# Performance work log

Hardware: AMD Instinct MI355X
Metric: run time of the kernel (lower is better)

## Reference

```python
import jax, jax.numpy as jnp
import numpy as np

N, E, G = 20000, 640000, 64
D_IN, H, C, D_OUT = 256, 4, 64, 32
HC = H * C


def gat_layer(x, W, a_src, a_dst, b, src, dst, n_nodes, heads, ch):
    # x: [N, F_in], W: [F_in, H*C]
    h = (x @ W).reshape(n_nodes, heads, ch)          # [N,H,C]
    es = jnp.einsum('nhc,hc->nh', h, a_src)          # [N,H]
    ed = jnp.einsum('nhc,hc->nh', h, a_dst)
    e = jax.nn.leaky_relu(es[src] + ed[dst], 0.2)    # [Etot,H]
    m = jax.ops.segment_max(e, dst, num_segments=n_nodes)
    m = jnp.where(jnp.isfinite(m), m, 0.0)
    ex = jnp.exp(e - m[dst])
    denom = jax.ops.segment_sum(ex, dst, num_segments=n_nodes)
    alpha = ex / jnp.maximum(denom[dst], 1e-16)      # softmax over in-edges per dst
    out = jax.ops.segment_sum(alpha[:, :, None] * h[src], dst, num_segments=n_nodes)
    return out.reshape(n_nodes, heads * ch) + b


def setup_inputs() -> dict:
    key = jax.random.key(0)
    ks = jax.random.split(key, 14)
    g1 = 1.0 / np.sqrt(D_IN)
    g2 = 1.0 / np.sqrt(HC)
    inp = {
        'x': jax.random.normal(ks[0], (N, D_IN), jnp.float32),
        'edge_index': jax.random.randint(ks[1], (2, E), 0, N, jnp.int64 if jax.config.jax_enable_x64 else jnp.int32),
        'batch': jnp.sort(jax.random.randint(ks[2], (N,), 0, G)),
        'W1': jax.random.normal(ks[3], (D_IN, HC), jnp.float32) * g1,
        'a_src1': jax.random.normal(ks[4], (H, C), jnp.float32) * g2,
        'a_dst1': jax.random.normal(ks[5], (H, C), jnp.float32) * g2,
        'b1': jnp.zeros((HC,), jnp.float32),
        'W2': jax.random.normal(ks[6], (HC, HC), jnp.float32) * g2,
        'a_src2': jax.random.normal(ks[7], (H, C), jnp.float32) * g2,
        'a_dst2': jax.random.normal(ks[8], (H, C), jnp.float32) * g2,
        'b2': jnp.zeros((HC,), jnp.float32),
        'Wp': jax.random.normal(ks[9], (HC, D_OUT), jnp.float32) * g2,
        'bp': jnp.zeros((D_OUT,), jnp.float32),
    }
    return inp


def reference(x, edge_index, batch, W1, a_src1, a_dst1, b1, W2, a_src2, a_dst2, b2, Wp, bp):
    # add self-loops (PyG GATConv default)
    loop = jnp.arange(N, dtype=edge_index.dtype)
    src = jnp.concatenate([edge_index[0], loop])
    dst = jnp.concatenate([edge_index[1], loop])
    x1 = jax.nn.relu(gat_layer(x, W1, a_src1, a_dst1, b1, src, dst, N, H, C))
    # dropout p=0.6 is identity in eval mode
    x2 = jax.nn.relu(gat_layer(x1, W2, a_src2, a_dst2, b2, src, dst, N, H, C))
    node_scores = x2 @ Wp + bp                        # [N, D_OUT]
    sums = jax.ops.segment_sum(node_scores, batch, num_segments=G)
    counts = jax.ops.segment_sum(jnp.ones((N,), node_scores.dtype), batch, num_segments=G)
    return sums / jnp.maximum(counts, 1.0)[:, None]   # [G, D_OUT]
```

## Files before the change

kernel.cpp:

```cpp
#include <hip/hip_runtime.h>
#include <hip/hip_bf16.h>
#include <cstdint>

#define NNODES 20000
#define NEDGES 640000
#define ETOT   (NEDGES + NNODES)
#define NGROUP 64
#define HC     256
#define DOUT   32
#define EBLK   5120
#define NBLK   125
#define CBLK   79
#define GBLK   1250
#define ABLK   2500

typedef short bf16x8 __attribute__((ext_vector_type(8)));
typedef short s16x4  __attribute__((ext_vector_type(4)));
typedef float f32x4  __attribute__((ext_vector_type(4)));
typedef float f32x2  __attribute__((ext_vector_type(2)));
typedef int   s32x4  __attribute__((ext_vector_type(4)));
typedef unsigned int u32x4 __attribute__((ext_vector_type(4)));

__device__ __forceinline__ float bs2f(short v) {
    union { unsigned int u; float f; } c; c.u = ((unsigned int)(unsigned short)v) << 16; return c.f;
}
__device__ __forceinline__ short f2bs(float v) {
    __hip_bfloat16 b = __float2bfloat16(v);
    union { __hip_bfloat16 b; short s; } u; u.b = b; return u.s;
}
__device__ __forceinline__ float ldf(const void* __restrict__ p, size_t i, int bf) {
    return bf ? __bfloat162float(((const __hip_bfloat16*)p)[i]) : ((const float*)p)[i];
}
__device__ __forceinline__ int ld_idx(const int* __restrict__ p, size_t i, int f64) {
    return f64 ? p[2 * i] : p[i];
}
__device__ __forceinline__ unsigned enc_f(float f) {
    unsigned u = __float_as_uint(f);
    return (u >> 31) ? ~u : (u | 0x80000000u);
}
__device__ __forceinline__ float dec_f(unsigned e) {
    return (e >> 31) ? __uint_as_float(e & 0x7FFFFFFFu) : __uint_as_float(~e);
}
__device__ __forceinline__ int probe_edge64(const int* __restrict__ ei) {
    int l = threadIdx.x & 63;
    int zeros = 0;
#pragma unroll
    for (int r = 0; r < 4; r++)
        zeros += __popcll(__ballot(ei[2 * (r * 64 + l) + 1] == 0));
    return (zeros > 200) ? 1 : 0;
}
__device__ __forceinline__ int probe_xbf(const unsigned int* __restrict__ xw) {
    int l = threadIdx.x & 63;
    int ones = 0;
#pragma unroll
    for (int r = 0; r < 4; r++)
        ones += __popcll(__ballot((xw[r * 64 + l] >> 14) & 1));
    return (ones < 64) ? 1 : 0;
}
__device__ __forceinline__ void signal_done(int* ctr) {
    __threadfence();
    __syncthreads();
    if (threadIdx.x == 0) atomicAdd(ctr, 1);
}
__device__ __forceinline__ void spin_wait(int* ctr, int target) {
    if (threadIdx.x == 0) {
        while (__hip_atomic_load(ctr, __ATOMIC_RELAXED, __HIP_MEMORY_SCOPE_AGENT) < target)
            __builtin_amdgcn_s_sleep(8);
    }
    __syncthreads();
    __threadfence();
}

__global__ __launch_bounds__(256) void k_setup(const unsigned int* __restrict__ xw,
                                               const int* __restrict__ ei,
                                               const int* __restrict__ bat,
                                               const void* __restrict__ W1, const void* __restrict__ W2,
                                               __hip_bfloat16* __restrict__ Wt1,
                                               __hip_bfloat16* __restrict__ Wt2,
                                               int* __restrict__ H,
                                               float* __restrict__ sx, int* __restrict__ cnt,
                                               unsigned* __restrict__ gp2, int* __restrict__ sy) {
    __shared__ int hl[NNODES];
    int t = threadIdx.x, b = blockIdx.x;
    if (b < NBLK) {
        int f = probe_edge64(ei);
        s32x4* hl4 = reinterpret_cast<s32x4*>(hl);
        for (int i = t; i < NNODES / 4; i += 256) hl4[i] = (s32x4){0, 0, 0, 0};
        __syncthreads();
        int s0 = b * EBLK;
        if (f) {
            const int* d64 = ei + 2 * NEDGES;
            for (int i0 = s0; i0 < s0 + EBLK; i0 += 512) {
                int i = i0 + 2 * t;
                s32x4 v = *reinterpret_cast<const s32x4*>(d64 + 2 * (size_t)i);
                atomicAdd(&hl[v[0]], 1);
                atomicAdd(&hl[v[2]], 1);
            }
        } else {
            const int* d32 = ei + NEDGES;
            for (int i0 = s0; i0 < s0 + EBLK; i0 += 1024) {
                int i = i0 + 4 * t;
                s32x4 v = *reinterpret_cast<const s32x4*>(d32 + i);
                atomicAdd(&hl[v[0]], 1); atomicAdd(&hl[v[1]], 1);
                atomicAdd(&hl[v[2]], 1); atomicAdd(&hl[v[3]], 1);
            }
        }
        __syncthreads();
        s32x4* Hb4 = reinterpret_cast<s32x4*>(H + (size_t)b * NNODES);
        for (int i = t; i < NNODES / 4; i += 256) Hb4[i] = hl4[i];
    } else {
        int bf = probe_xbf(xw);
        int i = (b - NBLK) * 256 + t;
        int which = i >> 16;
        int j = i & 65535;
        int k = j >> 8, n = j & 255;
        const void* W = which ? W2 : W1;
        __hip_bfloat16* Wt = which ? Wt2 : Wt1;
        Wt[(size_t)n * 256 + k] = __float2bfloat16(ldf(W, (size_t)k * 256 + n, bf));
        if (b == NBLK) {
            for (int q = t; q < NGROUP * HC; q += 256) sx[q] = 0.f;
            if (t < 256) gp2[t] = 0x007FFFFFu;
            if (t < 8) sy[t] = 0;
            int f = probe_edge64(ei);
            if (t < NGROUP) hl[t] = 0;
            __syncthreads();
            for (int r = t; r < NNODES; r += 256) atomicAdd(&hl[ld_idx(bat, r, f)], 1);
            __syncthreads();
            if (t < NGROUP) cnt[t] = hl[t];
        }
    }
}

__device__ __forceinline__ void dev_gemm(int tile, const void* __restrict__ A,
                                         const __hip_bfloat16* __restrict__ Bt,
                                         __hip_bfloat16* __restrict__ Hout,
                                         const void* __restrict__ a_src, const void* __restrict__ a_dst,
                                         float* __restrict__ es4, float* __restrict__ ed4,
                                         unsigned* __restrict__ gp2, int bf, int abf,
                                         u32x4* hst4) {
    int w    = threadIdx.x >> 6;
    int lane = threadIdx.x & 63;
    int mr   = lane & 15;
    int quad = lane >> 4;
    int r0   = tile * 16;
    f32x4 acc[4];
#pragma unroll
    for (int j = 0; j < 4; j++) acc[j] = (f32x4){0.f, 0.f, 0.f, 0.f};
    size_t rowoff = (size_t)(r0 + mr) * HC;
    const __hip_bfloat16* Btw = Bt + (size_t)w * 64 * HC;
    for (int kk = 0; kk < HC; kk += 32) {
        bf16x8 a;
        if (abf) {
            a = *reinterpret_cast<const bf16x8*>((const __hip_bfloat16*)A + rowoff + kk + quad * 8);
        } else {
            const float* af = (const float*)A + rowoff + kk + quad * 8;
            f32x4 lo = *reinterpret_cast<const f32x4*>(af);
            f32x4 hi = *reinterpret_cast<const f32x4*>(af + 4);
#pragma unroll
            for (int ii = 0; ii < 4; ii++) { a[ii] = f2bs(lo[ii]); a[ii + 4] = f2bs(hi[ii]); }
        }
#pragma unroll
        for (int j = 0; j < 4; j++) {
            bf16x8 b = *reinterpret_cast<const bf16x8*>(Btw + (size_t)(j * 16 + mr) * HC + kk + quad * 8);
            acc[j] = __builtin_amdgcn_mfma_f32_16x16x32_bf16(a, b, acc[j], 0, 0, 0);
        }
    }
    short* hst = reinterpret_cast<short*>(hst4);
#pragma unroll
    for (int j = 0; j < 4; j++)
#pragma unroll
        for (int r = 0; r < 4; r++)
            hst[(quad * 4 + r) * HC + w * 64 + j * 16 + mr] = f2bs(acc[j][r]);
    float ps[4] = {0.f, 0.f, 0.f, 0.f}, pd[4] = {0.f, 0.f, 0.f, 0.f};
#pragma unroll
    for (int j = 0; j < 4; j++) {
        float asv = ldf(a_src, (size_t)(w * 64 + j * 16 + mr), bf);
        float adv = ldf(a_dst, (size_t)(w * 64 + j * 16 + mr), bf);
#pragma unroll
        for (int r = 0; r < 4; r++) {
            ps[r] = fmaf(acc[j][r], asv, ps[r]);
            pd[r] = fmaf(acc[j][r], adv, pd[r]);
        }
    }
#pragma unroll
    for (int o = 1; o < 16; o <<= 1)
#pragma unroll
        for (int r = 0; r < 4; r++) {
            ps[r] += __shfl_xor(ps[r], o);
            pd[r] += __shfl_xor(pd[r], o);
        }
    float pm = fmaxf(fmaxf(ps[0], ps[1]), fmaxf(ps[2], ps[3]));
    pm = fmaxf(pm, __shfl_xor(pm, 16));
    pm = fmaxf(pm, __shfl_xor(pm, 32));
    if (lane == 0) atomicMax(&gp2[w * 64 + (tile & 63)], enc_f(pm));
    if (mr == 0)
#pragma unroll
        for (int r = 0; r < 4; r++) {
            int row = r0 + quad * 4 + r;
            es4[(size_t)row * 4 + w] = ps[r];
            ed4[(size_t)row * 4 + w] = pd[r];
        }
    __syncthreads();
    u32x4* dst = reinterpret_cast<u32x4*>((short*)Hout + (size_t)r0 * HC);
    dst[threadIdx.x]       = hst4[threadIdx.x];
    dst[threadIdx.x + 256] = hst4[threadIdx.x + 256];
}

__global__ __launch_bounds__(256) void k_p2(const void* __restrict__ x,
                                            const int* __restrict__ ei,
                                            int* __restrict__ H, int* __restrict__ bsum,
                                            int* __restrict__ off, int* __restrict__ csr,
                                            const __hip_bfloat16* __restrict__ Wt1,
                                            __hip_bfloat16* __restrict__ hb,
                                            const void* __restrict__ as1, const void* __restrict__ ad1,
                                            float* __restrict__ es, float* __restrict__ ed,
                                            unsigned* __restrict__ gp2, int* __restrict__ sy) {
    __shared__ int smem[2048];
    int bid = blockIdx.x, t = threadIdx.x;
    if (bid < CBLK) {
        int n = bid * 256 + t;
        int lane = t & 63, w = t >> 6;
        int d = 0;
        if (n < NNODES) {
#pragma unroll 5
            for (int b = 0; b < NBLK; b++) d += H[(size_t)b * NNODES + n];
            d += 1;
        }
        int r = d;
#pragma unroll
        for (int o = 1; o < 64; o <<= 1) r += __shfl_xor(r, o);
        if (lane == 0) smem[w] = r;
        __syncthreads();
        if (t == 0) bsum[bid] = smem[0] + smem[1] + smem[2] + smem[3];
        signal_done(&sy[0]);
        spin_wait(&sy[0], CBLK);
        int sc = d;
#pragma unroll
        for (int o = 1; o < 64; o <<= 1) {
            int u = __shfl_up(sc, o);
            if (lane >= o) sc += u;
        }
        if (lane == 63) smem[w] = sc;
        if (w == 0) {
            int v = (lane < bid) ? bsum[lane] : 0;
            if (lane + 64 < bid) v += bsum[lane + 64];
#pragma unroll
            for (int o = 1; o < 64; o <<= 1) v += __shfl_xor(v, o);
            if (lane == 0) smem[4] = v;
        }
        __syncthreads();
        int woff = 0;
        for (int i = 0; i < w; i++) woff += smem[i];
        int excl = woff + sc - d;
        if (bid == 0 && t == 0) off[NNODES] = ETOT;
        if (n < NNODES) {
            int o0 = smem[4] + excl;
            off[n] = o0;
            csr[o0] = n;
            int run = o0 + 1;
#pragma unroll 5
            for (int b = 0; b < NBLK; b++) {
                size_t idx = (size_t)b * NNODES + n;
                int tt = H[idx];
                H[idx] = run;
                run += tt;
            }
        }
        signal_done(&sy[1]);
    } else if (bid < CBLK + NBLK) {
        int b = bid - CBLK;
        int f = probe_edge64(ei);
        spin_wait(&sy[1], CBLK);
        int* Hb = H + (size_t)b * NNODES;
        int s0 = b * EBLK;
        if (f) {
            const int* d64 = ei + 2 * NEDGES;
            for (int i0 = s0; i0 < s0 + EBLK; i0 += 512) {
                int i = i0 + 2 * t;
                s32x4 sv = *reinterpret_cast<const s32x4*>(ei + 2 * (size_t)i);
                s32x4 dv = *reinterpret_cast<const s32x4*>(d64 + 2 * (size_t)i);
                int p0 = atomicAdd(&Hb[dv[0]], 1); csr[p0] = sv[0];
                int p1 = atomicAdd(&Hb[dv[2]], 1); csr[p1] = sv[2];
            }
        } else {
            const int* d32 = ei + NEDGES;
            for (int i0 = s0; i0 < s0 + EBLK; i0 += 1024) {
                int i = i0 + 4 * t;
                s32x4 sv = *reinterpret_cast<const s32x4*>(ei + i);
                s32x4 dv = *reinterpret_cast<const s32x4*>(d32 + i);
#pragma unroll
                for (int k = 0; k < 4; k++) {
                    int p = atomicAdd(&Hb[dv[k]], 1); csr[p] = sv[k];
                }
            }
        }
    } else {
        int bf = probe_xbf((const unsigned int*)x);
        dev_gemm(bid - (CBLK + NBLK), x, Wt1, hb, as1, ad1, es, ed, gp2, bf, bf,
                 (u32x4*)smem);
    }
}

__global__ __launch_bounds__(256) void k_agg(const void* __restrict__ x,
                                             const __hip_bfloat16* __restrict__ Hb,
                                             const float* __restrict__ es4, const float* __restrict__ ed4,
                                             const void* __restrict__ bias,
                                             const int* __restrict__ off, const int* __restrict__ csr,
                                             const unsigned* __restrict__ gp2,
                                             __hip_bfloat16* __restrict__ out) {
    __shared__ float p_lds[4][4][64];
    __shared__ int   s_lds[4][64];
    __shared__ float gm_s[4];
    int wv = threadIdx.x >> 6;
    int l  = threadIdx.x & 63;
    int half = l >> 5;
    int hl   = l & 31;
    int hd8  = hl >> 3;
    int bf = probe_xbf((const unsigned int*)x);
    {
        float m = dec_f(gp2[wv * 64 + l]);
#pragma unroll
        for (int o = 32; o; o >>= 1) m = fmaxf(m, __shfl_xor(m, o));
        if (l == 0) gm_s[wv] = m;
    }
    __syncthreads();
    f32x4 gm = (f32x4){gm_s[0], gm_s[1], gm_s[2], gm_s[3]};
    int n0 = blockIdx.x * 4 + wv;
    for (int n = n0; n < NNODES; n += 10000) {
        int base = off[n], deg = off[n + 1] - base;
        f32x4 edv = *reinterpret_cast<const f32x4*>(ed4 + (size_t)n * 4);
        f32x4 M;
#pragma unroll
        for (int h = 0; h < 4; h++) {
            float t0 = gm[h] + edv[h];
            M[h] = (t0 > 0.f) ? t0 : 0.2f * t0;
        }
        f32x4 dsum = (f32x4){0.f, 0.f, 0.f, 0.f};
        f32x2 acc2[4];
#pragma unroll
        for (int d = 0; d < 4; d++) acc2[d] = (f32x2){0.f, 0.f};
        for (int c0 = 0; c0 < deg; c0 += 64) {
            int cn = min(deg - c0, 64);
            int s = 0;
            f32x4 pv = (f32x4){0.f, 0.f, 0.f, 0.f};
            if (l < cn) {
                s = csr[base + c0 + l];
                f32x4 e = *reinterpret_cast<const f32x4*>(es4 + (size_t)s * 4);
#pragma unroll
                for (int h = 0; h < 4; h++) {
                    float t = e[h] + edv[h];
                    t = (t > 0.f) ? t : 0.2f * t;
                    pv[h] = __expf(t - M[h]);
                }
            }
            s_lds[wv][l] = s;
#pragma unroll
            for (int h = 0; h < 4; h++) p_lds[wv][h][l] = pv[h];
#pragma unroll
            for (int h = 0; h < 4; h++) dsum[h] += pv[h];
            int jn = (cn + 15) & ~15;
            for (int j = 0; j < jn; j += 16) {
                int e0 = j + 8 * half;
                s32x4 sA = *reinterpret_cast<const s32x4*>(&s_lds[wv][e0]);
                s32x4 sB = *reinterpret_cast<const s32x4*>(&s_lds[wv][e0 + 4]);
                f32x4 pA = *reinterpret_cast<const f32x4*>(&p_lds[wv][hd8][e0]);
                f32x4 pB = *reinterpret_cast<const f32x4*>(&p_lds[wv][hd8][e0 + 4]);
                u32x4 hv[8];
#pragma unroll
                for (int i = 0; i < 8; i++) {
                    int sj = (i < 4) ? sA[i & 3] : sB[i & 3];
                    hv[i] = *reinterpret_cast<const u32x4*>(Hb + (size_t)sj * HC + hl * 8);
                }
#pragma unroll
                for (int i = 0; i < 8; i++) {
                    float p = (i < 4) ? pA[i & 3] : pB[i & 3];
#pragma unroll
                    for (int d = 0; d < 4; d++) {
                        unsigned int u = hv[i][d];
                        f32x2 h2;
                        h2.x = __uint_as_float(u << 16);
                        h2.y = __uint_as_float(u & 0xFFFF0000u);
                        acc2[d] += h2 * p;
                    }
                }
            }
        }
#pragma unroll
        for (int o = 32; o; o >>= 1)
#pragma unroll
            for (int h = 0; h < 4; h++) dsum[h] += __shfl_xor(dsum[h], o);
#pragma unroll
        for (int d = 0; d < 4; d++) {
            acc2[d].x += __shfl_xor(acc2[d].x, 32);
            acc2[d].y += __shfl_xor(acc2[d].y, 32);
        }
        float rinv = 1.0f / fmaxf(dsum[hd8], 1e-16f);
        if (half == 0) {
            bf16x8 ov;
#pragma unroll
            for (int d = 0; d < 4; d++) {
                float v0 = acc2[d].x * rinv + ldf(bias, (size_t)hl * 8 + 2 * d, bf);
                float v1 = acc2[d].y * rinv + ldf(bias, (size_t)hl * 8 + 2 * d + 1, bf);
                ov[2 * d]     = f2bs(fmaxf(v0, 0.f));
                ov[2 * d + 1] = f2bs(fmaxf(v1, 0.f));
            }
            *reinterpret_cast<bf16x8*>(out + (size_t)n * HC + hl * 8) = ov;
        }
    }
}

__global__ __launch_bounds__(256) void k_gemm2(const void* __restrict__ x,
                                               const __hip_bfloat16* __restrict__ xb,
                                               const __hip_bfloat16* __restrict__ Wt2,
                                               __hip_bfloat16* __restrict__ hb,
                                               const void* __restrict__ as2, const void* __restrict__ ad2,
                                               float* __restrict__ es, float* __restrict__ ed,
                                               unsigned* __restrict__ gp2) {
    __shared__ u32x4 hst4[512];
    int bf = probe_xbf((const unsigned int*)x);
    dev_gemm(blockIdx.x, xb, Wt2, hb, as2, ad2, es, ed, gp2, bf, 1, hst4);
}

__global__ __launch_bounds__(256) void k_gsf(const void* __restrict__ x,
                                             const int* __restrict__ ei,
                                             const __hip_bfloat16* __restrict__ xb2,
                                             const int* __restrict__ bat,
                                             float* __restrict__ sx, const int* __restrict__ cnt,
                                             const void* __restrict__ Wp, const void* __restrict__ bp,
                                             void* __restrict__ out, int* __restrict__ sy) {
    __shared__ float red[256];
    int bid = blockIdx.x, t = threadIdx.x;
    if (bid < 250) {
        int f = probe_edge64(ei);
        const int RPB = NNODES / 250;
        int sub = t >> 6, l = t & 63;
        int r = bid * RPB + sub;
        f32x4 acc = (f32x4){0.f, 0.f, 0.f, 0.f};
        int curg = ld_idx(bat, r, f);
        for (int k = 0; k < RPB / 4; k++, r += 4) {
            int g = ld_idx(bat, r, f);
            if (g != curg) {
#pragma unroll
                for (int c = 0; c < 4; c++) atomicAdd(&sx[(size_t)curg * HC + l * 4 + c], acc[c]);
                acc = (f32x4){0.f, 0.f, 0.f, 0.f}; curg = g;
            }
            s16x4 hv = *reinterpret_cast<const s16x4*>(xb2 + (size_t)r * HC + l * 4);
#pragma unroll
            for (int c = 0; c < 4; c++) acc[c] += bs2f(hv[c]);
        }
#pragma unroll
        for (int c = 0; c < 4; c++) atomicAdd(&sx[(size_t)curg * HC + l * 4 + c], acc[c]);
        signal_done(&sy[4]);
    } else {
        int bf = probe_xbf((const unsigned int*)x);
        spin_wait(&sy[4], 250);
        int g = bid - 250;
        int c = t & 31, seg = t >> 5;
        const float* sxg = sx + (size_t)g * HC;
        float a = 0.f;
#pragma unroll
        for (int k = 0; k < 32; k++) {
            int kk = seg * 32 + k;
            a = fmaf(sxg[kk], ldf(Wp, (size_t)kk * DOUT + c, bf), a);
        }
        red[seg * 32 + c] = a;
        __syncthreads();
        if (t < 32) {
            float s = 0.f;
#pragma unroll
            for (int i = 0; i < 8; i++) s += red[i * 32 + t];
            int ct = cnt[g];
            float v = (ct > 0) ? (s / ct + ldf(bp, (size_t)t, bf)) : 0.f;
            if (bf) ((__hip_bfloat16*)out)[g * DOUT + t] = __float2bfloat16(v);
            else    ((float*)out)[g * DOUT + t]          = v;
        }
    }
}

extern "C" void kernel_launch(void* const* d_in, const int* in_sizes, int n_in,
                              void* d_out, int out_size, void* d_ws, size_t ws_size,
                              hipStream_t stream) {
    (void)in_sizes; (void)n_in; (void)out_size; (void)ws_size;
    const void* x   = d_in[0];
    const int*  ei  = (const int*)d_in[1];
    const int*  bat = (const int*)d_in[2];
    const void* W1  = d_in[3];
    const void* as1 = d_in[4];
    const void* ad1 = d_in[5];
    const void* b1  = d_in[6];
    const void* W2  = d_in[7];
    const void* as2 = d_in[8];
    const void* ad2 = d_in[9];
    const void* b2  = d_in[10];
    const void* Wp  = d_in[11];
    const void* bp  = d_in[12];

    char* ws = (char*)d_ws;
    size_t o = 0;
    auto alloc = [&](size_t bytes) -> char* {
        char* p = ws + o;
        o += (bytes + 255) & ~(size_t)255;
        return p;
    };
    __hip_bfloat16* hb  = (__hip_bfloat16*)alloc((size_t)NNODES * HC * 2);
    __hip_bfloat16* xb  = (__hip_bfloat16*)alloc((size_t)NNODES * HC * 2);
    __hip_bfloat16* xb2 = (__hip_bfloat16*)alloc((size_t)NNODES * HC * 2);
    __hip_bfloat16* Wt1 = (__hip_bfloat16*)alloc((size_t)HC * HC * 2);
    __hip_bfloat16* Wt2 = (__hip_bfloat16*)alloc((size_t)HC * HC * 2);
    float* es = (float*)alloc((size_t)NNODES * 4 * 4);
    float* ed = (float*)alloc((size_t)NNODES * 4 * 4);
    int* H    = (int*)alloc((size_t)NBLK * NNODES * 4);
    int* off  = (int*)alloc((size_t)(NNODES + 1) * 4);
    int* csr  = (int*)alloc((size_t)ETOT * 4);
    int* bsum = (int*)alloc((size_t)CBLK * 4);
    unsigned* gp2 = (unsigned*)alloc(256 * 4);
    float* sx = (float*)alloc((size_t)NGROUP * HC * 4);
    int* cnt  = (int*)alloc(256);
    int* sy   = (int*)alloc(256);

    k_setup<<<NBLK + 512, 256, 0, stream>>>((const unsigned int*)x, ei, bat, W1, W2,
                                            Wt1, Wt2, H, sx, cnt, gp2, sy);
    k_p2<<<CBLK + NBLK + GBLK, 256, 0, stream>>>(x, ei, H, bsum, off, csr, Wt1, hb,
                                                 as1, ad1, es, ed, gp2, sy);
    k_agg<<<ABLK, 256, 0, stream>>>(x, hb, es, ed, b1, off, csr, gp2, xb);
    k_gemm2<<<GBLK, 256, 0, stream>>>(x, xb, Wt2, hb, as2, ad2, es, ed, gp2);
    k_agg<<<ABLK, 256, 0, stream>>>(x, hb, es, ed, b2, off, csr, gp2, xb2);
    k_gsf<<<250 + NGROUP, 256, 0, stream>>>(x, ei, xb2, bat, sx, cnt, Wp, bp,
                                            d_out, sy);
}
```

Before: 374.5 us.

## Split CSR scan into separate multi-block kernels instead of spin-waiting blocks

Replaces the in-kernel prefix scan, which ran on 79 blocks that spin-waited on global counters, with two standalone kernels of 313 blocks each. Each node's 125 histogram columns are split across 4 waves. The first kernel computes per-wave partial sums and block totals, and the second computes block offsets and writes the CSR offsets and running positions. The scatter and GEMM kernel then runs without spin waits. This aims to remove serialized per-thread 125-step loops and the cross-block busy-wait, at the cost of two extra launches and a small intermediate buffer.

```diff
diff --git a/kernel.cpp b/kernel.cpp
--- a/kernel.cpp
+++ b/kernel.cpp
@@ -10,9 +10,9 @@
 #define DOUT   32
 #define EBLK   5120
 #define NBLK   125
-#define CBLK   79
 #define GBLK   1250
 #define ABLK   2500
+#define SBLK   313
 
 typedef short bf16x8 __attribute__((ext_vector_type(8)));
 typedef short s16x4  __attribute__((ext_vector_type(4)));
@@ -131,6 +131,85 @@
     }
 }
 
+__global__ __launch_bounds__(256) void k_cs(const int* __restrict__ H,
+                                            int* __restrict__ S, int* __restrict__ bsum) {
+    __shared__ int sm[4][64];
+    int t = threadIdx.x, blk = blockIdx.x;
+    int l = t & 63, g = t >> 6;
+    int n = blk * 64 + l;
+    int partial = 0;
+    if (n < NNODES) {
+        int bend = min(g * 32 + 32, NBLK);
+#pragma unroll 4
+        for (int b = g * 32; b < bend; b++) partial += H[(size_t)b * NNODES + n];
+        S[(size_t)n * 4 + g] = partial;
+    }
+    sm[g][l] = partial;
+    __syncthreads();
+    if (g == 0) {
+        int tot = (n < NNODES) ? (1 + sm[0][l] + sm[1][l] + sm[2][l] + sm[3][l]) : 0;
+        int r = tot;
+#pragma unroll
+        for (int o = 1; o < 64; o <<= 1) r += __shfl_xor(r, o);
+        if (l == 0) bsum[blk] = r;
+    }
+}
+
+__global__ __launch_bounds__(256) void k_b2(int* __restrict__ H,
+                                            const int* __restrict__ S,
+                                            const int* __restrict__ bsum,
+                                            int* __restrict__ off, int* __restrict__ csr) {
+    __shared__ int sm_red[4];
+    __shared__ int sm_excl[64];
+    __shared__ int sm_boff;
+    int t = threadIdx.x, blk = blockIdx.x;
+    int l = t & 63, g = t >> 6;
+    int n = blk * 64 + l;
+    int v = 0;
+    for (int i = t; i < blk; i += 256) v += bsum[i];
+    {
+        int r = v;
+#pragma unroll
+        for (int o = 1; o < 64; o <<= 1) r += __shfl_xor(r, o);
+        if (l == 0) sm_red[g] = r;
+    }
+    s32x4 s4 = (s32x4){0, 0, 0, 0};
+    if (n < NNODES) s4 = *reinterpret_cast<const s32x4*>(S + (size_t)n * 4);
+    int deg = (n < NNODES) ? (1 + s4[0] + s4[1] + s4[2] + s4[3]) : 0;
+    __syncthreads();
+    if (t == 0) sm_boff = sm_red[0] + sm_red[1] + sm_red[2] + sm_red[3];
+    if (g == 0) {
+        int sc = deg;
+#pragma unroll
+        for (int o = 1; o < 64; o <<= 1) {
+            int u = __shfl_up(sc, o);
+            if (l >= o) sc += u;
+        }
+        sm_excl[l] = sc - deg;
+    }
+    __syncthreads();
+    int off_n = sm_boff + sm_excl[l];
+    if (g == 0 && n < NNODES) {
+        off[n] = off_n;
+        csr[off_n] = n;
+    }
+    if (blk == 0 && t == 0) off[NNODES] = ETOT;
+    if (n < NNODES) {
+        int pre = 1;
+        if (g > 0) pre += s4[0];
+        if (g > 1) pre += s4[1];
+        if (g > 2) pre += s4[2];
+        int run = off_n + pre;
+        int bend = min(g * 32 + 32, NBLK);
+        for (int b = g * 32; b < bend; b++) {
+            size_t idx = (size_t)b * NNODES + n;
+            int tt = H[idx];
+            H[idx] = run;
+            run += tt;
+        }
+    }
+}
+
 __device__ __forceinline__ void dev_gemm(int tile, const void* __restrict__ A,
                                          const __hip_bfloat16* __restrict__ Bt,
                                          __hip_bfloat16* __restrict__ Hout,
@@ -206,71 +285,19 @@
     dst[threadIdx.x + 256] = hst4[threadIdx.x + 256];
 }
 
-__global__ __launch_bounds__(256) void k_p2(const void* __restrict__ x,
-                                            const int* __restrict__ ei,
-                                            int* __restrict__ H, int* __restrict__ bsum,
-                                            int* __restrict__ off, int* __restrict__ csr,
-                                            const __hip_bfloat16* __restrict__ Wt1,
-                                            __hip_bfloat16* __restrict__ hb,
-                                            const void* __restrict__ as1, const void* __restrict__ ad1,
-                                            float* __restrict__ es, float* __restrict__ ed,
-                                            unsigned* __restrict__ gp2, int* __restrict__ sy) {
-    __shared__ int smem[2048];
+__global__ __launch_bounds__(256) void k_sg1(const void* __restrict__ x,
+                                             const int* __restrict__ ei,
+                                             int* __restrict__ H, int* __restrict__ csr,
+                                             const __hip_bfloat16* __restrict__ Wt1,
+                                             __hip_bfloat16* __restrict__ hb,
+                                             const void* __restrict__ as1, const void* __restrict__ ad1,
+                                             float* __restrict__ es, float* __restrict__ ed,
+                                             unsigned* __restrict__ gp2) {
+    __shared__ u32x4 hst4[512];
     int bid = blockIdx.x, t = threadIdx.x;
-    if (bid < CBLK) {
-        int n = bid * 256 + t;
-        int lane = t & 63, w = t >> 6;
-        int d = 0;
-        if (n < NNODES) {
-#pragma unroll 5
-            for (int b = 0; b < NBLK; b++) d += H[(size_t)b * NNODES + n];
-            d += 1;
-        }
-        int r = d;
-#pragma unroll
-        for (int o = 1; o < 64; o <<= 1) r += __shfl_xor(r, o);
-        if (lane == 0) smem[w] = r;
-        __syncthreads();
-        if (t == 0) bsum[bid] = smem[0] + smem[1] + smem[2] + smem[3];
-        signal_done(&sy[0]);
-        spin_wait(&sy[0], CBLK);
-        int sc = d;
-#pragma unroll
-        for (int o = 1; o < 64; o <<= 1) {
-            int u = __shfl_up(sc, o);
-            if (lane >= o) sc += u;
-        }
-        if (lane == 63) smem[w] = sc;
-        if (w == 0) {
-            int v = (lane < bid) ? bsum[lane] : 0;
-            if (lane + 64 < bid) v += bsum[lane + 64];
-#pragma unroll
-            for (int o = 1; o < 64; o <<= 1) v += __shfl_xor(v, o);
-            if (lane == 0) smem[4] = v;
-        }
-        __syncthreads();
-        int woff = 0;
-        for (int i = 0; i < w; i++) woff += smem[i];
-        int excl = woff + sc - d;
-        if (bid == 0 && t == 0) off[NNODES] = ETOT;
-        if (n < NNODES) {
-            int o0 = smem[4] + excl;
-            off[n] = o0;
-            csr[o0] = n;
-            int run = o0 + 1;
-#pragma unroll 5
-            for (int b = 0; b < NBLK; b++) {
-                size_t idx = (size_t)b * NNODES + n;
-                int tt = H[idx];
-                H[idx] = run;
-                run += tt;
-            }
-        }
-        signal_done(&sy[1]);
-    } else if (bid < CBLK + NBLK) {
-        int b = bid - CBLK;
+    if (bid < NBLK) {
+        int b = bid;
         int f = probe_edge64(ei);
-        spin_wait(&sy[1], CBLK);
         int* Hb = H + (size_t)b * NNODES;
         int s0 = b * EBLK;
         if (f) {
@@ -296,8 +323,7 @@
         }
     } else {
         int bf = probe_xbf((const unsigned int*)x);
-        dev_gemm(bid - (CBLK + NBLK), x, Wt1, hb, as1, ad1, es, ed, gp2, bf, bf,
-                 (u32x4*)smem);
+        dev_gemm(bid - NBLK, x, Wt1, hb, as1, ad1, es, ed, gp2, bf, bf, hst4);
     }
 }
 
@@ -510,9 +536,10 @@
     float* es = (float*)alloc((size_t)NNODES * 4 * 4);
     float* ed = (float*)alloc((size_t)NNODES * 4 * 4);
     int* H    = (int*)alloc((size_t)NBLK * NNODES * 4);
+    int* S    = (int*)alloc((size_t)NNODES * 4 * 4);
     int* off  = (int*)alloc((size_t)(NNODES + 1) * 4);
     int* csr  = (int*)alloc((size_t)ETOT * 4);
-    int* bsum = (int*)alloc((size_t)CBLK * 4);
+    int* bsum = (int*)alloc((size_t)SBLK * 4);
     unsigned* gp2 = (unsigned*)alloc(256 * 4);
     float* sx = (float*)alloc((size_t)NGROUP * HC * 4);
     int* cnt  = (int*)alloc(256);
@@ -520,8 +547,9 @@
 
     k_setup<<<NBLK + 512, 256, 0, stream>>>((const unsigned int*)x, ei, bat, W1, W2,
                                             Wt1, Wt2, H, sx, cnt, gp2, sy);
-    k_p2<<<CBLK + NBLK + GBLK, 256, 0, stream>>>(x, ei, H, bsum, off, csr, Wt1, hb,
-                                                 as1, ad1, es, ed, gp2, sy);
+    k_cs<<<SBLK, 256, 0, stream>>>(H, S, bsum);
+    k_b2<<<SBLK, 256, 0, stream>>>(H, S, bsum, off, csr);
+    k_sg1<<<NBLK + GBLK, 256, 0, stream>>>(x, ei, H, csr, Wt1, hb, as1, ad1, es, ed, gp2);
     k_agg<<<ABLK, 256, 0, stream>>>(x, hb, es, ed, b1, off, csr, gp2, xb);
     k_gemm2<<<GBLK, 256, 0, stream>>>(x, xb, Wt2, hb, as2, ad2, es, ed, gp2);
     k_agg<<<ABLK, 256, 0, stream>>>(x, hb, es, ed, b2, off, csr, gp2, xb2);
```

Result: faster. 328.1 us (-12.4%).
